# Optimization experiments

Hardware: AMD Instinct MI355X
Metric: run time of the kernel (lower is better)

## Reference

```python
import jax, jax.numpy as jnp
import numpy as np

E = 8  # path_num


def setup_inputs() -> dict:
    key = jax.random.key(0)
    k1, k2, k3 = jax.random.split(key, 3)
    N, D = 8192, 1024
    x = jax.random.normal(k1, (N, D), dtype=jnp.float32)
    hot_mask = jax.random.randint(k2, (N, E), 0, 2, dtype=jnp.int32)  # multi-hot 0/1
    score = jax.random.uniform(k3, (N, E), dtype=jnp.float32)
    return {"x": x, "hot_mask": hot_mask, "score": score}


def reference(x, hot_mask, score):
    # MoE dispatch (route_logic='1d', transform=True):
    # for each expert e, gather tokens n with hot_mask[n, e] == 1 in order,
    # scaled by score[n, e]. Outputs padded to capacity N (zeros beyond count).
    N, D = x.shape
    mask = hot_mask > 0                                   # [N, E]
    ranks = jnp.cumsum(hot_mask, axis=0) - 1              # [N, E] position within expert
    dest = jnp.where(mask, ranks, N)                      # dropped tokens -> dump slot N
    tags = jnp.arange(N, dtype=jnp.int64)                 # flow_tag (arange via pack_invalid_flow)
    scale = score * mask.astype(score.dtype)              # [N, E]

    def per_expert(dest_e, scale_e, mask_e):
        vals = x * scale_e[:, None]                       # [N, D] scaled (zero if not routed)
        out = jnp.zeros((N + 1, D), x.dtype).at[dest_e].add(vals)[:N]
        tag_out = jnp.zeros((N + 1,), jnp.int64).at[dest_e].add(
            jnp.where(mask_e, tags, 0))[:N]               # gathered out_flow_tag, 0-padded
        return out, tag_out

    out_data, out_tags = jax.vmap(per_expert, in_axes=(1, 1, 1))(dest, scale, mask)
    counts = jnp.sum(hot_mask, axis=0)                    # [E] tokens per expert
    return out_data, out_tags, counts
```

## Files before the change

kernel.cpp:

```cpp
#include <hip/hip_runtime.h>

#define N_TOK 8192
#define D_DIM 1024
#define E_NUM 8
#define D4 (D_DIM / 4)
#define SCAN_BLOCKS 32

typedef unsigned long long u64;
typedef float f32x4 __attribute__((ext_vector_type(4)));


__device__ __forceinline__ u64 pack4(const int4 a) {
    return (u64)a.x | ((u64)a.y << 16) | ((u64)a.z << 32) | ((u64)a.w << 48);
}

__global__ __launch_bounds__(256) void scan_all_kernel(
    const int4* __restrict__ mask4,
    int* __restrict__ dest,
    int* __restrict__ counts_i,
    float* __restrict__ out_tags,
    float* __restrict__ out_counts)
{
    const int bid = blockIdx.x;
    const int t   = threadIdx.x;
    const int n   = bid * 256 + t;

    u64 pre_lo = 0, pre_hi = 0, all_lo = 0, all_hi = 0, my_lo = 0, my_hi = 0;
    for (int k = 0; k < SCAN_BLOCKS; ++k) {
        const int tok = k * 256 + t;
        const u64 lo = pack4(mask4[(size_t)tok * 2]);
        const u64 hi = pack4(mask4[(size_t)tok * 2 + 1]);
        all_lo += lo; all_hi += hi;
        if (k < bid)  { pre_lo += lo; pre_hi += hi; }
        if (k == bid) { my_lo  = lo; my_hi  = hi; }
    }

    __shared__ u64 s1[256], s2[256];

    s1[t] = all_lo; s2[t] = all_hi; __syncthreads();
    for (int off = 128; off > 0; off >>= 1) {
        if (t < off) { s1[t] += s1[t + off]; s2[t] += s2[t + off]; }
        __syncthreads();
    }
    const u64 tot_lo = s1[0], tot_hi = s2[0];
    __syncthreads();

    s1[t] = pre_lo; s2[t] = pre_hi; __syncthreads();
    for (int off = 128; off > 0; off >>= 1) {
        if (t < off) { s1[t] += s1[t + off]; s2[t] += s2[t + off]; }
        __syncthreads();
    }
    const u64 base_lo = s1[0], base_hi = s2[0];
    __syncthreads();

    s1[t] = my_lo; s2[t] = my_hi; __syncthreads();
    for (int off = 1; off < 256; off <<= 1) {
        u64 p1 = 0, p2 = 0;
        if (t >= off) { p1 = s1[t - off]; p2 = s2[t - off]; }
        __syncthreads();
        if (t >= off) { s1[t] += p1; s2[t] += p2; }
        __syncthreads();
    }
    const u64 plo = (s1[t] - my_lo) + base_lo;
    const u64 phi = (s2[t] - my_hi) + base_hi;

    int d[8];
    #pragma unroll
    for (int e = 0; e < E_NUM; ++e) {
        const int sh = 16 * (e & 3);
        const int m  = (int)(((e < 4 ? my_lo : my_hi) >> sh) & 0xFFFF);
        const int r  = (int)(((e < 4 ? plo   : phi  ) >> sh) & 0xFFFF);
        d[e] = m ? r : -1;
        if (m) out_tags[(size_t)e * N_TOK + r] = (float)n;
    }

    int4* dest4 = (int4*)dest;
    int4 d0; d0.x = d[0]; d0.y = d[1]; d0.z = d[2]; d0.w = d[3];
    int4 d1; d1.x = d[4]; d1.y = d[5]; d1.z = d[6]; d1.w = d[7];
    dest4[(size_t)n * 2]     = d0;
    dest4[(size_t)n * 2 + 1] = d1;

    int cnt[8];
    #pragma unroll
    for (int e = 0; e < E_NUM; ++e) {
        cnt[e] = (int)(((e < 4 ? tot_lo : tot_hi) >> (16 * (e & 3))) & 0xFFFF);
    }
    if (bid == 0 && t < E_NUM) {
        counts_i[t]   = cnt[t];
        out_counts[t] = (float)cnt[t];
    }
    #pragma unroll
    for (int e = 0; e < E_NUM; ++e) {
        const int idx = cnt[e] + n;
        if (idx < N_TOK) out_tags[(size_t)e * N_TOK + idx] = 0.0f;
    }
}

__global__ __launch_bounds__(256) void dispatch_scatter_kernel(
    const f32x4* __restrict__ x,
    const float* __restrict__ score,
    const int* __restrict__ dest,
    const int* __restrict__ counts_i,
    f32x4* __restrict__ out)
{
    const int b = blockIdx.x;
    const int c = threadIdx.x;

    if (b < N_TOK) {
        const int n = b;
        const f32x4 xv = x[(size_t)n * D4 + c];
        #pragma unroll
        for (int e = 0; e < E_NUM; ++e) {
            const int r = dest[(size_t)n * E_NUM + e];
            if (r >= 0) {
                const float s = score[(size_t)n * E_NUM + e];
                const f32x4 v = xv * s;
                __builtin_nontemporal_store(
                    v, &out[((size_t)e * N_TOK + r) * D4 + c]);
            }
        }
    } else {
        const int row = b - N_TOK;
        const int e   = row >> 13;
        const int r   = row & (N_TOK - 1);
        if (r >= counts_i[e]) {
            const f32x4 z = (f32x4)0.0f;
            __builtin_nontemporal_store(z, &out[(size_t)row * D4 + c]);
        }
    }
}

extern "C" void kernel_launch(void* const* d_in, const int* in_sizes, int n_in,
                              void* d_out, int out_size, void* d_ws, size_t ws_size,
                              hipStream_t stream) {
    const float* x        = (const float*)d_in[0];
    const int*   hot_mask = (const int*)d_in[1];
    const float* score    = (const float*)d_in[2];

    float* out        = (float*)d_out;
    float* out_data   = out;
    float* out_tags   = out + (size_t)E_NUM * N_TOK * D_DIM;
    float* out_counts = out_tags + (size_t)E_NUM * N_TOK;

    int* dest     = (int*)d_ws;
    int* counts_i = dest + (size_t)N_TOK * E_NUM;

    scan_all_kernel<<<SCAN_BLOCKS, 256, 0, stream>>>(
        (const int4*)hot_mask, dest, counts_i, out_tags, out_counts);

    dispatch_scatter_kernel<<<N_TOK + E_NUM * N_TOK, 256, 0, stream>>>(
        (const f32x4*)x, score, dest, counts_i, (f32x4*)out_data);
}
```

Baseline: 60.53 us.

## Use wave shuffles in scan, vectorize dest/score loads, compact zero-padding grid

The scan kernel's LDS tree reductions and block-wide prefix scan are replaced by 64-lane shuffle scans and reductions, with a small LDS exchange across the four waves. The scatter kernel reads the eight dest and score values per token as two int4/float4 loads each instead of scalar per-expert loads. The zero-padding part of the grid drops from one block per output row (65536 blocks, most of which exit early) to 1024 blocks per expert, each zeroing 8 consecutive rows starting at that expert's count. This removes a large number of empty block launches, at the cost of fewer rows per block being spread across the GPU.

```diff
diff --git a/kernel.cpp b/kernel.cpp
--- a/kernel.cpp
+++ b/kernel.cpp
@@ -5,6 +5,8 @@
 #define E_NUM 8
 #define D4 (D_DIM / 4)
 #define SCAN_BLOCKS 32
+#define PAD_BLOCKS_PER_E 1024
+#define PAD_ROWS 8
 
 typedef unsigned long long u64;
 typedef float f32x4 __attribute__((ext_vector_type(4)));
@@ -21,9 +23,11 @@
     float* __restrict__ out_tags,
     float* __restrict__ out_counts)
 {
-    const int bid = blockIdx.x;
-    const int t   = threadIdx.x;
-    const int n   = bid * 256 + t;
+    const int bid  = blockIdx.x;
+    const int t    = threadIdx.x;
+    const int lane = t & 63;
+    const int wave = t >> 6;
+    const int n    = bid * 256 + t;
 
     u64 pre_lo = 0, pre_hi = 0, all_lo = 0, all_hi = 0, my_lo = 0, my_hi = 0;
     for (int k = 0; k < SCAN_BLOCKS; ++k) {
@@ -35,34 +39,43 @@
         if (k == bid) { my_lo  = lo; my_hi  = hi; }
     }
 
-    __shared__ u64 s1[256], s2[256];
+    u64 sc_lo = my_lo, sc_hi = my_hi;
+    #pragma unroll
+    for (int off = 1; off < 64; off <<= 1) {
+        const u64 a = __shfl_up(sc_lo, off, 64);
+        const u64 b = __shfl_up(sc_hi, off, 64);
+        if (lane >= off) { sc_lo += a; sc_hi += b; }
+    }
+    const u64 wsum_lo = __shfl(sc_lo, 63, 64);
+    const u64 wsum_hi = __shfl(sc_hi, 63, 64);
 
-    s1[t] = all_lo; s2[t] = all_hi; __syncthreads();
-    for (int off = 128; off > 0; off >>= 1) {
-        if (t < off) { s1[t] += s1[t + off]; s2[t] += s2[t + off]; }
-        __syncthreads();
+    u64 asum_lo = all_lo, asum_hi = all_hi, psum_lo = pre_lo, psum_hi = pre_hi;
+    #pragma unroll
+    for (int off = 1; off < 64; off <<= 1) {
+        asum_lo += __shfl_xor(asum_lo, off, 64);
+        asum_hi += __shfl_xor(asum_hi, off, 64);
+        psum_lo += __shfl_xor(psum_lo, off, 64);
+        psum_hi += __shfl_xor(psum_hi, off, 64);
     }
-    const u64 tot_lo = s1[0], tot_hi = s2[0];
+
+    __shared__ u64 lds[4][6];
+    if (lane == 0) {
+        lds[wave][0] = wsum_lo; lds[wave][1] = wsum_hi;
+        lds[wave][2] = asum_lo; lds[wave][3] = asum_hi;
+        lds[wave][4] = psum_lo; lds[wave][5] = psum_hi;
+    }
     __syncthreads();
 
-    s1[t] = pre_lo; s2[t] = pre_hi; __syncthreads();
-    for (int off = 128; off > 0; off >>= 1) {
-        if (t < off) { s1[t] += s1[t + off]; s2[t] += s2[t + off]; }
-        __syncthreads();
+    u64 tot_lo = 0, tot_hi = 0, base_lo = 0, base_hi = 0, woff_lo = 0, woff_hi = 0;
+    #pragma unroll
+    for (int w = 0; w < 4; ++w) {
+        tot_lo  += lds[w][2]; tot_hi  += lds[w][3];
+        base_lo += lds[w][4]; base_hi += lds[w][5];
+        if (w < wave) { woff_lo += lds[w][0]; woff_hi += lds[w][1]; }
     }
-    const u64 base_lo = s1[0], base_hi = s2[0];
-    __syncthreads();
 
-    s1[t] = my_lo; s2[t] = my_hi; __syncthreads();
-    for (int off = 1; off < 256; off <<= 1) {
-        u64 p1 = 0, p2 = 0;
-        if (t >= off) { p1 = s1[t - off]; p2 = s2[t - off]; }
-        __syncthreads();
-        if (t >= off) { s1[t] += p1; s2[t] += p2; }
-        __syncthreads();
-    }
-    const u64 plo = (s1[t] - my_lo) + base_lo;
-    const u64 phi = (s2[t] - my_hi) + base_hi;
+    const u64 plo = (sc_lo - my_lo) + woff_lo + base_lo;
+    const u64 phi = (sc_hi - my_hi) + woff_hi + base_hi;
 
     int d[8];
     #pragma unroll
@@ -109,23 +122,36 @@
     if (b < N_TOK) {
         const int n = b;
         const f32x4 xv = x[(size_t)n * D4 + c];
+        const int4 da = ((const int4*)dest)[(size_t)n * 2];
+        const int4 db = ((const int4*)dest)[(size_t)n * 2 + 1];
+        const float4 sa = ((const float4*)score)[(size_t)n * 2];
+        const float4 sb = ((const float4*)score)[(size_t)n * 2 + 1];
+        const int   de[8] = { da.x, da.y, da.z, da.w, db.x, db.y, db.z, db.w };
+        const float se[8] = { sa.x, sa.y, sa.z, sa.w, sb.x, sb.y, sb.z, sb.w };
+
         #pragma unroll
         for (int e = 0; e < E_NUM; ++e) {
-            const int r = dest[(size_t)n * E_NUM + e];
+            const int r = de[e];
             if (r >= 0) {
-                const float s = score[(size_t)n * E_NUM + e];
-                const f32x4 v = xv * s;
+                const f32x4 v = xv * se[e];
                 __builtin_nontemporal_store(
                     v, &out[((size_t)e * N_TOK + r) * D4 + c]);
             }
         }
     } else {
-        const int row = b - N_TOK;
-        const int e   = row >> 13;
-        const int r   = row & (N_TOK - 1);
-        if (r >= counts_i[e]) {
-            const f32x4 z = (f32x4)0.0f;
-            __builtin_nontemporal_store(z, &out[(size_t)row * D4 + c]);
+        const int p  = b - N_TOK;
+        const int e  = p >> 10;
+        const int k  = p & (PAD_BLOCKS_PER_E - 1);
+        const int r0 = counts_i[e] + k * PAD_ROWS;
+        if (r0 >= N_TOK) return;
+        const f32x4 z = (f32x4)0.0f;
+        #pragma unroll
+        for (int i = 0; i < PAD_ROWS; ++i) {
+            const int r = r0 + i;
+            if (r < N_TOK) {
+                __builtin_nontemporal_store(
+                    z, &out[((size_t)e * N_TOK + r) * D4 + c]);
+            }
         }
     }
 }
@@ -148,6 +174,6 @@
     scan_all_kernel<<<SCAN_BLOCKS, 256, 0, stream>>>(
         (const int4*)hot_mask, dest, counts_i, out_tags, out_counts);
 
-    dispatch_scatter_kernel<<<N_TOK + E_NUM * N_TOK, 256, 0, stream>>>(
+    dispatch_scatter_kernel<<<N_TOK + E_NUM * PAD_BLOCKS_PER_E, 256, 0, stream>>>(
         (const f32x4*)x, score, dest, counts_i, (f32x4*)out_data);
 }
```

Measured after the change: 64.99 us. 7.4% more time.
